# Kernel optimization log

Hardware: AMD Instinct MI355X
Metric: run time of the kernel (lower is better)

The kernel has to match this reference:

```python
import jax, jax.numpy as jnp
import numpy as np
from jax import lax

G = 31      # grid_size
C = 16      # c (representative feature dim)
NL = 16     # n_L representative colors
CP = 128    # c_prime
S = G + 1   # corner-point spatial size = 32


def _conv(x, w, b):
    # 3x3 stride-1 pad-1 conv, NCHW / OIHW
    y = lax.conv_general_dilated(x, w, (1, 1), 'SAME',
                                 dimension_numbers=('NCHW', 'OIHW', 'NCHW'))
    return y + b[None, :, None, None]


def _bn(x, gamma, beta, mean, var):
    # eval-mode BatchNorm2d
    inv = gamma / jnp.sqrt(var + 1e-5)
    return x * inv[None, :, None, None] + (beta - mean * inv)[None, :, None, None]


def _block(x, w1, b1, g, be, m, v, w2, b2):
    # convBnSwish (stride=1) followed by plain 3x3 conv
    h = _conv(x, w1, b1)
    h = _bn(h, g, be, m, v)
    h = h * jax.nn.sigmoid(h)  # SiLU
    return _conv(h, w2, b2)


def setup_inputs() -> dict:
    key = jax.random.key(0)
    ks = jax.random.split(key, 16)
    B = 8
    d = {
        'f': jax.random.normal(ks[0], (B, C, 496, 496), jnp.float32),
        'features': jax.random.normal(ks[1], (B, CP, S, S), jnp.float32),
        # convR_L params
        'wR1': jax.random.normal(ks[2], (CP, CP, 3, 3), jnp.float32) * 0.03,
        'bR1': jnp.zeros((CP,), jnp.float32),
        'gR': jnp.ones((CP,), jnp.float32),
        'betR': jnp.zeros((CP,), jnp.float32),
        'mR': jax.random.normal(ks[3], (CP,), jnp.float32) * 0.1,
        'vR': jax.random.uniform(ks[4], (CP,), jnp.float32, 0.5, 1.5),
        'wR2': jax.random.normal(ks[5], (C * NL, CP, 3, 3), jnp.float32) * 0.03,
        'bR2': jnp.zeros((C * NL,), jnp.float32),
        # convT_L params
        'wT1': jax.random.normal(ks[6], (CP, CP, 3, 3), jnp.float32) * 0.03,
        'bT1': jnp.zeros((CP,), jnp.float32),
        'gT': jnp.ones((CP,), jnp.float32),
        'betT': jnp.zeros((CP,), jnp.float32),
        'mT': jax.random.normal(ks[7], (CP,), jnp.float32) * 0.1,
        'vT': jax.random.uniform(ks[8], (CP,), jnp.float32, 0.5, 1.5),
        'wT2': jax.random.normal(ks[9], (3 * NL, CP, 3, 3), jnp.float32) * 0.03,
        'bT2': jnp.zeros((3 * NL,), jnp.float32),
    }
    return d


def _corners(x):
    # x: [B,S,S,d,NL] -> concat 4 grid-cell corner points along color axis -> [B,G,G,d,4*NL]
    return jnp.concatenate([x[:, :-1, :-1], x[:, 1:, :-1],
                            x[:, :-1, 1:], x[:, 1:, 1:]], axis=-1)


def reference(f, features, wR1, bR1, gR, betR, mR, vR, wR2, bR2,
              wT1, bT1, gT, betT, mT, vT, wT2, bT2):
    B, _, H, W = f.shape
    hp, wp = H // G, W // G  # H,W chosen as multiples of G so padding() is a no-op

    r = _block(features, wR1, bR1, gR, betR, mR, vR, wR2, bR2)  # [B, C*NL, S, S]
    t = _block(features, wT1, bT1, gT, betT, mT, vT, wT2, bT2)  # [B, 3*NL, S, S]
    r = r.reshape(B, C, NL, S, S).transpose(0, 3, 4, 1, 2)      # [B,S,S,C,NL]
    t = t.reshape(B, 3, NL, S, S).transpose(0, 3, 4, 1, 2)      # [B,S,S,3,NL]

    r4 = _corners(r)  # [B,G,G,C,4NL]
    t4 = _corners(t)  # [B,G,G,3,4NL]

    # split f into GxG patches of (hp,wp): [B,G,G,hp*wp,C]
    fp = f.reshape(B, C, G, hp, G, wp).transpose(0, 2, 4, 3, 5, 1)
    fp = fp.reshape(B, G, G, hp * wp, C)

    scores = jnp.einsum('bijpc,bijcn->bijpn', fp, r4) / np.sqrt(C).astype(np.float32)
    att = jax.nn.softmax(scores, axis=-1)                        # [B,G,G,hp*wp,4NL]
    y = jnp.einsum('bijpn,bijdn->bijpd', att, t4)                # [B,G,G,hp*wp,3]
    y = y.reshape(B, G, G, hp, wp, 3).transpose(0, 5, 1, 3, 2, 4).reshape(B, 3, H, W)
    return y
```

## Files before the change

kernel.cpp:

```cpp
#include <hip/hip_runtime.h>
#include <hip/hip_bf16.h>
#include <stdint.h>
#include <stddef.h>

using u32 = unsigned int;
using u16 = unsigned short;

typedef short bf16x8 __attribute__((ext_vector_type(8)));
typedef _Float16 f16x8 __attribute__((ext_vector_type(8)));
typedef float f32x4 __attribute__((ext_vector_type(4)));
typedef u32  u32x4 __attribute__((ext_vector_type(4)));

__device__ __forceinline__ u16 f2bf(float f) {
  u32 u = __builtin_bit_cast(u32, f);
  u32 r = (u + 0x7FFFu + ((u >> 16) & 1u)) >> 16;
  return (u16)r;
}

__global__ __launch_bounds__(256) void repack_kernel(
    const float* wR1, const float* wT1, const float* wR2, const float* wT2,
    const float* bR1, const float* gR, const float* betR, const float* mR, const float* vR,
    const float* bT1, const float* gT, const float* betT, const float* mT, const float* vT,
    const float* bR2, const float* bT2,
    u16* wb1, u16* wb2, float* scale1, float* shift1, float* biasC)
{
  if (blockIdx.x == 2592) {
    int t = threadIdx.x;
    float g, v, be, mm, bb;
    if (t < 128) { g = gR[t]; v = vR[t]; be = betR[t]; mm = mR[t]; bb = bR1[t]; }
    else         { g = gT[t-128]; v = vT[t-128]; be = betT[t-128]; mm = mT[t-128]; bb = bT1[t-128]; }
    float sc = g * rsqrtf(v + 1e-5f);
    scale1[t] = sc;
    shift1[t] = (bb - mm) * sc + be;
    biasC[t] = bR2[t];
    if (t < 64) biasC[256 + t] = (t < 48) ? bT2[t] : 0.0f;
    return;
  }
  int idx = blockIdx.x * 256 + threadIdx.x;
  if (idx < 294912) {
    int oc = idx / 1152, k = idx - oc * 1152;
    int tap = k >> 7, ic = k & 127;
    float w = (oc < 128) ? wR1[(oc * 128 + ic) * 9 + tap]
                         : wT1[((oc - 128) * 128 + ic) * 9 + tap];
    wb1[idx] = f2bf(w);
  } else {
    int r2 = idx - 294912;
    int oc = r2 / 1152, k = r2 - oc * 1152;
    int tap = k >> 7, ic = k & 127;
    float w;
    if (oc < 256)            w = wR2[(oc * 128 + ic) * 9 + tap];
    else if (oc - 256 < 48)  w = wT2[((oc - 256) * 128 + ic) * 9 + tap];
    else                     w = 0.0f;
    wb2[r2] = f2bf(w);
  }
}

__global__ __launch_bounds__(256) void transpose_kernel(const float* feat, u16* feat_t)
{
  __shared__ float tile[128 * 33];
  int b = blockIdx.x >> 5, y = blockIdx.x & 31;
  int t = threadIdx.x;
  const float* src = feat + (size_t)(b * 128) * 1024 + y * 32;
#pragma unroll
  for (int q = 0; q < 16; q++) {
    int idx = q * 256 + t;
    int ic = idx >> 5, x = idx & 31;
    tile[ic * 33 + x] = src[(size_t)ic * 1024 + x];
  }
  __syncthreads();
  u16* dst = feat_t + (size_t)((b * 32 + y) * 32) * 128;
#pragma unroll
  for (int q = 0; q < 16; q++) {
    int idx = q * 256 + t;
    int x = idx >> 7, ic = idx & 127;
    dst[x * 128 + ic] = f2bf(tile[ic * 33 + x]);
  }
}

template <int SRCC, int EPI>
__global__ __launch_bounds__(256) void conv_gemm_kernel(
    const u16* __restrict__ src, const u16* __restrict__ Bt,
    u16* __restrict__ out0, float* __restrict__ out1,
    const float* __restrict__ c0, const float* __restrict__ c1)
{
  __shared__ u16 As[128 * 40];
  __shared__ u16 Bs[64 * 40];
  int t = threadIdx.x;
  int lane = t & 63, wid = t >> 6;
  int wm = wid >> 1, wn = wid & 1;
  int Mbase = blockIdx.x * 128, Nbase = blockIdx.y * 64;
  int icOff = (EPI == 1 && blockIdx.y == 4) ? 128 : 0;

  int rA = t >> 2, chA = t & 3;
  int p0 = Mbase + rA, p1 = p0 + 64;
  int y0 = (p0 >> 5) & 31, x0 = p0 & 31;
  int y1 = (p1 >> 5) & 31, x1 = p1 & 31;
  const u16* aSrc0 = src + (size_t)p0 * SRCC + icOff + chA * 8;
  const u16* aSrc1 = src + (size_t)p1 * SRCC + icOff + chA * 8;
  u16* aDst0 = &As[rA * 40 + chA * 8];
  u16* aDst1 = &As[(rA + 64) * 40 + chA * 8];
  const u16* bSrc = Bt + (size_t)(Nbase + rA) * 1152 + chA * 8;
  u16* bDst = &Bs[rA * 40 + chA * 8];

  f32x4 acc[4][2] = {};
  for (int kt = 0; kt < 36; kt++) {
    int tap = kt >> 2, icr = (kt & 3) * 32;
    int dy = tap / 3 - 1, dx = tap - (tap / 3) * 3 - 1;
    int aoff = (dy * 32 + dx) * SRCC + icr;
    __syncthreads();
    u32x4 v0 = {}, v1 = {};
    if ((u32)(y0 + dy) < 32u && (u32)(x0 + dx) < 32u)
      v0 = *reinterpret_cast<const u32x4*>(aSrc0 + (ptrdiff_t)aoff);
    if ((u32)(y1 + dy) < 32u && (u32)(x1 + dx) < 32u)
      v1 = *reinterpret_cast<const u32x4*>(aSrc1 + (ptrdiff_t)aoff);
    u32x4 vb = *reinterpret_cast<const u32x4*>(bSrc + kt * 32);
    *reinterpret_cast<u32x4*>(aDst0) = v0;
    *reinterpret_cast<u32x4*>(aDst1) = v1;
    *reinterpret_cast<u32x4*>(bDst) = vb;
    __syncthreads();
    int ko = (lane >> 4) * 8;
    bf16x8 af[4], bfr[2];
#pragma unroll
    for (int mt = 0; mt < 4; mt++)
      af[mt] = *reinterpret_cast<const bf16x8*>(&As[(wm * 64 + mt * 16 + (lane & 15)) * 40 + ko]);
#pragma unroll
    for (int nt = 0; nt < 2; nt++)
      bfr[nt] = *reinterpret_cast<const bf16x8*>(&Bs[(wn * 32 + nt * 16 + (lane & 15)) * 40 + ko]);
#pragma unroll
    for (int mt = 0; mt < 4; mt++)
#pragma unroll
      for (int nt = 0; nt < 2; nt++)
        acc[mt][nt] = __builtin_amdgcn_mfma_f32_16x16x32_bf16(af[mt], bfr[nt], acc[mt][nt], 0, 0, 0);
  }
#pragma unroll
  for (int mt = 0; mt < 4; mt++) {
#pragma unroll
    for (int nt = 0; nt < 2; nt++) {
      int col = Nbase + wn * 32 + nt * 16 + (lane & 15);
#pragma unroll
      for (int r = 0; r < 4; r++) {
        int rowp = Mbase + wm * 64 + mt * 16 + (lane >> 4) * 4 + r;
        float v = acc[mt][nt][r];
        if (EPI == 0) {
          float yv = v * c0[col] + c1[col];
          float h = yv / (1.0f + __expf(-yv));
          out0[(size_t)rowp * 256 + col] = f2bf(h);
        } else {
          float rv = v + c0[col];
          if (col < 256) {
            reinterpret_cast<_Float16*>(out0)[(size_t)rowp * 256 + (col & 15) * 16 + (col >> 4)] =
                (_Float16)(rv * 0.125f);
          } else {
            int cT = col - 256;
            if (cT < 48) out1[(size_t)rowp * 64 + (cT & 15) * 4 + (cT >> 4)] = rv;
            else         out1[(size_t)rowp * 64 + (cT & 15) * 4 + 3] = 0.0f;
          }
        }
      }
    }
  }
}

__global__ __launch_bounds__(256) void attn_kernel(
    const float* __restrict__ f, const _Float16* __restrict__ rbuf,
    const float* __restrict__ tbuf, float* __restrict__ out)
{
  const size_t cs = (size_t)496 * 496;
  int blk = blockIdx.x;
  int b = blk / 961, rem = blk - b * 961;
  int i = rem / 31, j = rem - i * 31;
  int t = threadIdx.x;
  int lane = t & 63, w = t >> 6;
  int q = lane >> 4, nl = lane & 15;

  f16x8 bfr[4]; float4 tq[4];
#pragma unroll
  for (int g = 0; g < 4; g++) {
    int ii = i + (g & 1), jj = j + (g >> 1);
    int pix = (b * 32 + ii) * 32 + jj;
    bfr[g] = *reinterpret_cast<const f16x8*>(rbuf + (size_t)pix * 256 + nl * 16 + (q & 1) * 8);
    tq[g] = reinterpret_cast<const float4*>(tbuf)[(size_t)pix * 16 + nl];
  }
  const float* fbase = f + ((size_t)b * 16 + (q & 1) * 8) * cs + (size_t)(i * 16) * 496 + j * 16 + nl;

#pragma unroll
  for (int mt = 0; mt < 4; mt++) {
    int py = w * 4 + mt;
    const float* fp = fbase + (size_t)py * 496;
    f16x8 afr;
#pragma unroll
    for (int c = 0; c < 8; c++) afr[c] = (_Float16)fp[(size_t)c * cs];
    f32x4 zero = {0.f, 0.f, 0.f, 0.f};
    f32x4 a0 = __builtin_amdgcn_mfma_f32_16x16x32_f16(afr, bfr[0], zero, 0, 0, 0);
    f32x4 a1 = __builtin_amdgcn_mfma_f32_16x16x32_f16(afr, bfr[1], zero, 0, 0, 0);
    f32x4 a2 = __builtin_amdgcn_mfma_f32_16x16x32_f16(afr, bfr[2], zero, 0, 0, 0);
    f32x4 a3 = __builtin_amdgcn_mfma_f32_16x16x32_f16(afr, bfr[3], zero, 0, 0, 0);
    float ls[4], yo0[4], yo1[4], yo2[4];
#pragma unroll
    for (int r = 0; r < 4; r++) {
      float e0 = __expf(a0[r]), e1 = __expf(a1[r]),
            e2 = __expf(a2[r]), e3 = __expf(a3[r]);
      ls[r]  = (e0 + e1) + (e2 + e3);
      yo0[r] = e0 * tq[0].x + e1 * tq[1].x + e2 * tq[2].x + e3 * tq[3].x;
      yo1[r] = e0 * tq[0].y + e1 * tq[1].y + e2 * tq[2].y + e3 * tq[3].y;
      yo2[r] = e0 * tq[0].z + e1 * tq[1].z + e2 * tq[2].z + e3 * tq[3].z;
    }
#pragma unroll
    for (int m2 = 1; m2 < 16; m2 <<= 1) {
#pragma unroll
      for (int r = 0; r < 4; r++) {
        ls[r]  += __shfl_xor(ls[r],  m2);
        yo0[r] += __shfl_xor(yo0[r], m2);
        yo1[r] += __shfl_xor(yo1[r], m2);
        yo2[r] += __shfl_xor(yo2[r], m2);
      }
    }
    if (nl < 3) {
      float* op = out + ((size_t)b * 3 + nl) * cs + (size_t)(i * 16 + py) * 496 + j * 16 + q * 4;
#pragma unroll
      for (int r = 0; r < 4; r++) {
        float yv = (nl == 0) ? yo0[r] : ((nl == 1) ? yo1[r] : yo2[r]);
        op[r] = yv * __builtin_amdgcn_rcpf(ls[r]);
      }
    }
  }
}

extern "C" void kernel_launch(void* const* d_in, const int* in_sizes, int n_in,
                              void* d_out, int out_size, void* d_ws, size_t ws_size,
                              hipStream_t stream)
{
  const float* f    = (const float*)d_in[0];
  const float* feats= (const float*)d_in[1];
  const float* wR1  = (const float*)d_in[2];
  const float* bR1  = (const float*)d_in[3];
  const float* gR   = (const float*)d_in[4];
  const float* betR = (const float*)d_in[5];
  const float* mR   = (const float*)d_in[6];
  const float* vR   = (const float*)d_in[7];
  const float* wR2  = (const float*)d_in[8];
  const float* bR2  = (const float*)d_in[9];
  const float* wT1  = (const float*)d_in[10];
  const float* bT1  = (const float*)d_in[11];
  const float* gT   = (const float*)d_in[12];
  const float* betT = (const float*)d_in[13];
  const float* mT   = (const float*)d_in[14];
  const float* vT   = (const float*)d_in[15];
  const float* wT2  = (const float*)d_in[16];
  const float* bT2  = (const float*)d_in[17];
  (void)in_sizes; (void)n_in; (void)out_size; (void)ws_size;

  char* ws = (char*)d_ws;
  u16*   wb1    = (u16*)(ws + 0);
  u16*   wb2    = (u16*)(ws + 589824);
  float* scale1 = (float*)(ws + 1327104);
  float* shift1 = scale1 + 256;
  float* biasC  = scale1 + 512;
  u16*   feat_t = (u16*)(ws + 1330432);
  u16*   hbuf   = (u16*)(ws + 3427584);
  u16*   rbuf16 = (u16*)(ws + 7621888);
  float* tbuf   = (float*)(ws + 11816192);

  repack_kernel<<<dim3(2593), dim3(256), 0, stream>>>(
      wR1, wT1, wR2, wT2, bR1, gR, betR, mR, vR, bT1, gT, betT, mT, vT,
      bR2, bT2, wb1, wb2, scale1, shift1, biasC);

  transpose_kernel<<<dim3(256), dim3(256), 0, stream>>>(feats, feat_t);

  conv_gemm_kernel<128, 0><<<dim3(64, 4), dim3(256), 0, stream>>>(
      feat_t, wb1, hbuf, nullptr, scale1, shift1);

  conv_gemm_kernel<256, 1><<<dim3(64, 5), dim3(256), 0, stream>>>(
      hbuf, wb2, rbuf16, tbuf, biasC, nullptr);

  attn_kernel<<<dim3(7688), dim3(256), 0, stream>>>(
      f, (const _Float16*)rbuf16, tbuf, (float*)d_out);
}
```

Baseline: 320.0 us.

## Stage f tile through LDS with vector loads and swap MFMA operand order in attention

The attention kernel now loads each 16x16x16 patch of f with coalesced float4 loads, packs channel pairs to fp16 and stores them in a swizzled LDS tile. This replaces the strided scalar per-channel global loads. The MFMA operands are swapped so pixels land on lanes, which reduces the cross-lane reduction to two shuffles and gives coalesced output stores. Softmax now subtracts the max, using exp2 with the log2e factor folded into the R scale. The conv GEMM also gets register prefetch of the next K tile and a K-chunk-major LDS layout, at the cost of more registers and some added LDS traffic.

```diff
diff --git a/kernel.cpp b/kernel.cpp
--- a/kernel.cpp
+++ b/kernel.cpp
@@ -10,6 +10,8 @@
 typedef _Float16 f16x8 __attribute__((ext_vector_type(8)));
 typedef float f32x4 __attribute__((ext_vector_type(4)));
 typedef u32  u32x4 __attribute__((ext_vector_type(4)));
+
+#define RSCALE 0.18033688011112042f
 
 __device__ __forceinline__ u16 f2bf(float f) {
   u32 u = __builtin_bit_cast(u32, f);
@@ -83,54 +85,61 @@
     u16* __restrict__ out0, float* __restrict__ out1,
     const float* __restrict__ c0, const float* __restrict__ c1)
 {
-  __shared__ u16 As[128 * 40];
-  __shared__ u16 Bs[64 * 40];
+  __shared__ u16 As[4 * 128 * 8];
+  __shared__ u16 Bs[4 * 64 * 8];
   int t = threadIdx.x;
   int lane = t & 63, wid = t >> 6;
   int wm = wid >> 1, wn = wid & 1;
   int Mbase = blockIdx.x * 128, Nbase = blockIdx.y * 64;
   int icOff = (EPI == 1 && blockIdx.y == 4) ? 128 : 0;
 
-  int rA = t >> 2, chA = t & 3;
+  int rA = t >> 2, kc = t & 3;
   int p0 = Mbase + rA, p1 = p0 + 64;
   int y0 = (p0 >> 5) & 31, x0 = p0 & 31;
   int y1 = (p1 >> 5) & 31, x1 = p1 & 31;
-  const u16* aSrc0 = src + (size_t)p0 * SRCC + icOff + chA * 8;
-  const u16* aSrc1 = src + (size_t)p1 * SRCC + icOff + chA * 8;
-  u16* aDst0 = &As[rA * 40 + chA * 8];
-  u16* aDst1 = &As[(rA + 64) * 40 + chA * 8];
-  const u16* bSrc = Bt + (size_t)(Nbase + rA) * 1152 + chA * 8;
-  u16* bDst = &Bs[rA * 40 + chA * 8];
-
-  f32x4 acc[4][2] = {};
-  for (int kt = 0; kt < 36; kt++) {
-    int tap = kt >> 2, icr = (kt & 3) * 32;
+  const u16* aSrc0 = src + (size_t)p0 * SRCC + icOff + kc * 8;
+  const u16* aSrc1 = src + (size_t)p1 * SRCC + icOff + kc * 8;
+  const u16* bSrc  = Bt + (size_t)(Nbase + rA) * 1152 + kc * 8;
+  u16* aDst0 = &As[kc * 1024 + rA * 8];
+  u16* aDst1 = &As[kc * 1024 + (rA + 64) * 8];
+  u16* bDst  = &Bs[kc * 512 + rA * 8];
+
+  u32x4 v0, v1, vb;
+  auto LOADK = [&](int kt) {
+    int tap = kt >> 2;
     int dy = tap / 3 - 1, dx = tap - (tap / 3) * 3 - 1;
-    int aoff = (dy * 32 + dx) * SRCC + icr;
-    __syncthreads();
-    u32x4 v0 = {}, v1 = {};
+    int aoff = (dy * 32 + dx) * SRCC + (kt & 3) * 32;
+    u32x4 z = {};
+    v0 = z; v1 = z;
     if ((u32)(y0 + dy) < 32u && (u32)(x0 + dx) < 32u)
       v0 = *reinterpret_cast<const u32x4*>(aSrc0 + (ptrdiff_t)aoff);
     if ((u32)(y1 + dy) < 32u && (u32)(x1 + dx) < 32u)
       v1 = *reinterpret_cast<const u32x4*>(aSrc1 + (ptrdiff_t)aoff);
-    u32x4 vb = *reinterpret_cast<const u32x4*>(bSrc + kt * 32);
+    vb = *reinterpret_cast<const u32x4*>(bSrc + kt * 32);
+  };
+
+  f32x4 acc[4][2] = {};
+  LOADK(0);
+  int L = lane & 15, qs = lane >> 4;
+  for (int kt = 0; kt < 36; kt++) {
+    __syncthreads();
     *reinterpret_cast<u32x4*>(aDst0) = v0;
     *reinterpret_cast<u32x4*>(aDst1) = v1;
-    *reinterpret_cast<u32x4*>(bDst) = vb;
+    *reinterpret_cast<u32x4*>(bDst)  = vb;
+    if (kt < 35) LOADK(kt + 1);
     __syncthreads();
-    int ko = (lane >> 4) * 8;
-    bf16x8 af[4], bfr[2];
+    bf16x8 af[4], bfr2[2];
 #pragma unroll
     for (int mt = 0; mt < 4; mt++)
-      af[mt] = *reinterpret_cast<const bf16x8*>(&As[(wm * 64 + mt * 16 + (lane & 15)) * 40 + ko]);
+      af[mt] = *reinterpret_cast<const bf16x8*>(&As[qs * 1024 + (wm * 64 + mt * 16 + L) * 8]);
 #pragma unroll
     for (int nt = 0; nt < 2; nt++)
-      bfr[nt] = *reinterpret_cast<const bf16x8*>(&Bs[(wn * 32 + nt * 16 + (lane & 15)) * 40 + ko]);
+      bfr2[nt] = *reinterpret_cast<const bf16x8*>(&Bs[qs * 512 + (wn * 32 + nt * 16 + L) * 8]);
 #pragma unroll
     for (int mt = 0; mt < 4; mt++)
 #pragma unroll
       for (int nt = 0; nt < 2; nt++)
-        acc[mt][nt] = __builtin_amdgcn_mfma_f32_16x16x32_bf16(af[mt], bfr[nt], acc[mt][nt], 0, 0, 0);
+        acc[mt][nt] = __builtin_amdgcn_mfma_f32_16x16x32_bf16(af[mt], bfr2[nt], acc[mt][nt], 0, 0, 0);
   }
 #pragma unroll
   for (int mt = 0; mt < 4; mt++) {
@@ -149,7 +158,7 @@
           float rv = v + c0[col];
           if (col < 256) {
             reinterpret_cast<_Float16*>(out0)[(size_t)rowp * 256 + (col & 15) * 16 + (col >> 4)] =
-                (_Float16)(rv * 0.125f);
+                (_Float16)(rv * RSCALE);
           } else {
             int cT = col - 256;
             if (cT < 48) out1[(size_t)rowp * 64 + (cT & 15) * 4 + (cT >> 4)] = rv;
@@ -163,9 +172,10 @@
 
 __global__ __launch_bounds__(256) void attn_kernel(
     const float* __restrict__ f, const _Float16* __restrict__ rbuf,
-    const float* __restrict__ tbuf, float* __restrict__ out)
+    const float4* __restrict__ tbuf, float* __restrict__ out)
 {
   const size_t cs = (size_t)496 * 496;
+  __shared__ u16 fl[4096];
   int blk = blockIdx.x;
   int b = blk / 961, rem = blk - b * 961;
   int i = rem / 31, j = rem - i * 31;
@@ -173,55 +183,80 @@
   int lane = t & 63, w = t >> 6;
   int q = lane >> 4, nl = lane & 15;
 
-  f16x8 bfr[4]; float4 tq[4];
+  {
+    int a = t >> 5;
+    int spy = (t >> 1) & 15;
+    int half = t & 1;
+    const float* fb = f + ((size_t)b * 16 + 2 * a) * cs
+                        + (size_t)(i * 16 + spy) * 496 + j * 16 + half * 8;
+    float4 c0a = *reinterpret_cast<const float4*>(fb);
+    float4 c0b = *reinterpret_cast<const float4*>(fb + 4);
+    float4 c1a = *reinterpret_cast<const float4*>(fb + cs);
+    float4 c1b = *reinterpret_cast<const float4*>(fb + cs + 4);
+    float lo[8] = {c0a.x, c0a.y, c0a.z, c0a.w, c0b.x, c0b.y, c0b.z, c0b.w};
+    float hi[8] = {c1a.x, c1a.y, c1a.z, c1a.w, c1b.x, c1b.y, c1b.z, c1b.w};
+    int base = spy * 256 + (a >> 2) * 128 + (a & 3) * 2;
+#pragma unroll
+    for (int p = 0; p < 8; p++) {
+      int px = half * 8 + p;
+      u32 pk = __builtin_bit_cast(u32, __builtin_amdgcn_cvt_pkrtz(lo[p], hi[p]));
+      *reinterpret_cast<u32*>(&fl[base + ((px ^ spy) * 8)]) = pk;
+    }
+  }
+
+  f16x8 bfr[4];
+  float tx[16], ty[16], tz[16];
 #pragma unroll
   for (int g = 0; g < 4; g++) {
     int ii = i + (g & 1), jj = j + (g >> 1);
     int pix = (b * 32 + ii) * 32 + jj;
     bfr[g] = *reinterpret_cast<const f16x8*>(rbuf + (size_t)pix * 256 + nl * 16 + (q & 1) * 8);
-    tq[g] = reinterpret_cast<const float4*>(tbuf)[(size_t)pix * 16 + nl];
-  }
-  const float* fbase = f + ((size_t)b * 16 + (q & 1) * 8) * cs + (size_t)(i * 16) * 496 + j * 16 + nl;
+#pragma unroll
+    for (int r = 0; r < 4; r++) {
+      float4 tv = tbuf[(size_t)pix * 16 + q * 4 + r];
+      tx[g * 4 + r] = tv.x; ty[g * 4 + r] = tv.y; tz[g * 4 + r] = tv.z;
+    }
+  }
+  __syncthreads();
 
 #pragma unroll
   for (int mt = 0; mt < 4; mt++) {
     int py = w * 4 + mt;
-    const float* fp = fbase + (size_t)py * 496;
-    f16x8 afr;
-#pragma unroll
-    for (int c = 0; c < 8; c++) afr[c] = (_Float16)fp[(size_t)c * cs];
-    f32x4 zero = {0.f, 0.f, 0.f, 0.f};
-    f32x4 a0 = __builtin_amdgcn_mfma_f32_16x16x32_f16(afr, bfr[0], zero, 0, 0, 0);
-    f32x4 a1 = __builtin_amdgcn_mfma_f32_16x16x32_f16(afr, bfr[1], zero, 0, 0, 0);
-    f32x4 a2 = __builtin_amdgcn_mfma_f32_16x16x32_f16(afr, bfr[2], zero, 0, 0, 0);
-    f32x4 a3 = __builtin_amdgcn_mfma_f32_16x16x32_f16(afr, bfr[3], zero, 0, 0, 0);
-    float ls[4], yo0[4], yo1[4], yo2[4];
+    f16x8 afr = *reinterpret_cast<const f16x8*>(&fl[py * 256 + (q & 1) * 128 + ((nl ^ py) & 15) * 8]);
+    f32x4 z = {0.f, 0.f, 0.f, 0.f};
+    f32x4 s0 = __builtin_amdgcn_mfma_f32_16x16x32_f16(bfr[0], afr, z, 0, 0, 0);
+    f32x4 s1 = __builtin_amdgcn_mfma_f32_16x16x32_f16(bfr[1], afr, z, 0, 0, 0);
+    f32x4 s2 = __builtin_amdgcn_mfma_f32_16x16x32_f16(bfr[2], afr, z, 0, 0, 0);
+    f32x4 s3 = __builtin_amdgcn_mfma_f32_16x16x32_f16(bfr[3], afr, z, 0, 0, 0);
+
+    float pm = s0[0];
 #pragma unroll
     for (int r = 0; r < 4; r++) {
-      float e0 = __expf(a0[r]), e1 = __expf(a1[r]),
-            e2 = __expf(a2[r]), e3 = __expf(a3[r]);
-      ls[r]  = (e0 + e1) + (e2 + e3);
-      yo0[r] = e0 * tq[0].x + e1 * tq[1].x + e2 * tq[2].x + e3 * tq[3].x;
-      yo1[r] = e0 * tq[0].y + e1 * tq[1].y + e2 * tq[2].y + e3 * tq[3].y;
-      yo2[r] = e0 * tq[0].z + e1 * tq[1].z + e2 * tq[2].z + e3 * tq[3].z;
-    }
-#pragma unroll
-    for (int m2 = 1; m2 < 16; m2 <<= 1) {
-#pragma unroll
-      for (int r = 0; r < 4; r++) {
-        ls[r]  += __shfl_xor(ls[r],  m2);
-        yo0[r] += __shfl_xor(yo0[r], m2);
-        yo1[r] += __shfl_xor(yo1[r], m2);
-        yo2[r] += __shfl_xor(yo2[r], m2);
-      }
-    }
-    if (nl < 3) {
-      float* op = out + ((size_t)b * 3 + nl) * cs + (size_t)(i * 16 + py) * 496 + j * 16 + q * 4;
-#pragma unroll
-      for (int r = 0; r < 4; r++) {
-        float yv = (nl == 0) ? yo0[r] : ((nl == 1) ? yo1[r] : yo2[r]);
-        op[r] = yv * __builtin_amdgcn_rcpf(ls[r]);
-      }
+      pm = fmaxf(pm, s0[r]); pm = fmaxf(pm, s1[r]);
+      pm = fmaxf(pm, s2[r]); pm = fmaxf(pm, s3[r]);
+    }
+    pm = fmaxf(pm, __shfl_xor(pm, 16));
+    pm = fmaxf(pm, __shfl_xor(pm, 32));
+
+    float l = 0.f, o0 = 0.f, o1 = 0.f, o2 = 0.f;
+#pragma unroll
+    for (int r = 0; r < 4; r++) {
+      float e0 = exp2f(s0[r] - pm), e1 = exp2f(s1[r] - pm),
+            e2 = exp2f(s2[r] - pm), e3 = exp2f(s3[r] - pm);
+      l  += (e0 + e1) + (e2 + e3);
+      o0 += e0 * tx[r] + e1 * tx[4 + r] + e2 * tx[8 + r] + e3 * tx[12 + r];
+      o1 += e0 * ty[r] + e1 * ty[4 + r] + e2 * ty[8 + r] + e3 * ty[12 + r];
+      o2 += e0 * tz[r] + e1 * tz[4 + r] + e2 * tz[8 + r] + e3 * tz[12 + r];
+    }
+    l  += __shfl_xor(l, 16);  l  += __shfl_xor(l, 32);
+    o0 += __shfl_xor(o0, 16); o0 += __shfl_xor(o0, 32);
+    o1 += __shfl_xor(o1, 16); o1 += __shfl_xor(o1, 32);
+    o2 += __shfl_xor(o2, 16); o2 += __shfl_xor(o2, 32);
+
+    if (q < 3) {
+      float yv = (q == 0) ? o0 : ((q == 1) ? o1 : o2);
+      out[((size_t)b * 3 + q) * cs + (size_t)(i * 16 + py) * 496 + j * 16 + nl] =
+          yv * __builtin_amdgcn_rcpf(l);
     }
   }
 }
@@ -274,5 +309,5 @@
       hbuf, wb2, rbuf16, tbuf, biasC, nullptr);
 
   attn_kernel<<<dim3(7688), dim3(256), 0, stream>>>(
-      f, (const _Float16*)rbuf16, tbuf, (float*)d_out);
-}
+      f, (const _Float16*)rbuf16, (const float4*)tbuf, (float*)d_out);
+}
```

Measured after the change: 291.3 us. -9.0%, faster.
